# Kernel optimization log

Hardware: AMD Instinct MI355X
Metric: run time of the kernel (lower is better)

## Reference

```python
import jax, jax.numpy as jnp
import numpy as np

ALPHA = 0.2  # LeakyReLU negative slope


def setup_inputs() -> dict:
    key = jax.random.key(0)
    k1, k2, k3, k4 = jax.random.split(key, 4)
    B, N, IN, OUT = 4, 512, 128, 64
    input_feature = jax.random.normal(k1, (B, N, IN), dtype=jnp.float32)
    adj = jax.random.randint(k2, (N, N), 0, 2, dtype=jnp.int32)
    # xavier_uniform with gain=1.414 (as in torch init)
    lim_W = 1.414 * np.sqrt(6.0 / (IN + OUT))
    W = jax.random.uniform(k3, (IN, OUT), minval=-lim_W, maxval=lim_W, dtype=jnp.float32)
    lim_a = 1.414 * np.sqrt(6.0 / (2 * OUT + 1))
    a = jax.random.uniform(k4, (2 * OUT, 1), minval=-lim_a, maxval=lim_a, dtype=jnp.float32)
    return {"input_feature": input_feature, "adj": adj, "W": W, "a": a}


def reference(input_feature, adj, W, a):
    B = input_feature.shape[0]
    N = adj.shape[0]
    h = jnp.matmul(input_feature, W)              # (B, N, out)
    out = h.shape[-1]
    # Faithful replication of the torch repeat/cat(dim=1)/view pattern.
    part1 = jnp.tile(h, (1, 1, N)).reshape(B, N * N, out)  # h.repeat(1,1,N).view
    part2 = jnp.tile(h, (1, N, 1))                          # h.repeat(1,N,1)
    a_input = jnp.concatenate([part1, part2], axis=1).reshape(B, N, N, 2 * out)
    e = jax.nn.leaky_relu(jnp.squeeze(jnp.matmul(a_input, a), -1), negative_slope=ALPHA)  # (B,N,N)
    # NOTE: source overwrites the adj-masked tensor with softmax(e) — mask is dead code.
    attention = jax.nn.softmax(e, axis=2)
    # dropout is a no-op in eval mode
    h_prime = jnp.matmul(attention, h)            # (B, N, out)
    return jax.nn.elu(h_prime)                    # concat=True -> elu
```

## Files before the change

kernel.cpp:

```cpp
#include <hip/hip_runtime.h>
#include <math.h>

#define ALPHA 0.2f


#define MAGIC_ARR 0x13579BDFu
#define MAGIC_DON 0x2468ACE0u

__device__ __forceinline__ unsigned ld_acq(unsigned* p) {
    return __hip_atomic_load(p, __ATOMIC_ACQUIRE, __HIP_MEMORY_SCOPE_AGENT);
}
__device__ __forceinline__ void st_rel(unsigned* p, unsigned v) {
    __hip_atomic_store(p, v, __ATOMIC_RELEASE, __HIP_MEMORY_SCOPE_AGENT);
}
__device__ __forceinline__ void st_rlx(unsigned* p, unsigned v) {
    __hip_atomic_store(p, v, __ATOMIC_RELAXED, __HIP_MEMORY_SCOPE_AGENT);
}
__device__ __forceinline__ float ldf(float* p) {
    return __hip_atomic_load(p, __ATOMIC_RELAXED, __HIP_MEMORY_SCOPE_AGENT);
}
__device__ __forceinline__ void stf(float* p, float v) {
    __hip_atomic_store(p, v, __ATOMIC_RELAXED, __HIP_MEMORY_SCOPE_AGENT);
}

__device__ __forceinline__ void wait16(unsigned* slots, unsigned magic, int lane) {
    for (;;) {
        unsigned v = (lane < 16) ? ld_acq(&slots[lane]) : magic;
        if (__all(v == magic)) return;
        __builtin_amdgcn_s_sleep(8);
    }
}

__global__ __launch_bounds__(256) void gat_v9(
    const float* __restrict__ X, const float* __restrict__ W,
    const float* __restrict__ a, float* __restrict__ out, float* __restrict__ ws)
{
    __shared__ float XB[32][132];
    __shared__ float wa1[128], wa2[128];
    __shared__ float a_s[128];
    __shared__ float p_s[32], q_s[32];
    __shared__ float ecl[16];
    __shared__ float xs_l[3][128];
    __shared__ float Sc[3][64];
    __shared__ float zsc;

    const int tid  = threadIdx.x;
    const int lane = tid & 63;
    const int b    = blockIdx.x >> 4;
    const int r    = blockIdx.x & 15;
    const float* Xb = X + b * 65536;

    float*    wsF  = ws + b * 8192;
    unsigned* arr  = (unsigned*)wsF;
    unsigned* dn   = (unsigned*)wsF + 16;
    float*    Zp   = wsF + 32;
    float*    xs0p = wsF + 64;
    float*    xs1p = wsF + 64 + 2048;
    float*    xtp  = wsF + 64 + 4096;

    const int k2 = tid >> 1, hf = tid & 1;
    const float4* wr = (const float4*)(W + k2 * 64 + hf * 32);
    float4 wv[8];
#pragma unroll
    for (int i = 0; i < 8; ++i) wv[i] = wr[i];

    const int ra = tid >> 3, oct = tid & 7;
    const float4* xrA = (const float4*)(Xb + (32 * r + ra) * 128 + oct * 16);
    float4 xa[4];
#pragma unroll
    for (int i = 0; i < 4; ++i) xa[i] = xrA[i];

    const int gi = (ra < 16) ? (16 * r + ra) : (256 + 16 * r + (ra - 16));
    const float4* xrB = (const float4*)(Xb + gi * 128 + oct * 16);
    float4 xb[4];
#pragma unroll
    for (int i = 0; i < 4; ++i) xb[i] = xrB[i];

    if (tid < 128) a_s[tid] = a[tid];
    __syncthreads();

    {
        float r1 = 0.f, r2 = 0.f;
#pragma unroll
        for (int i = 0; i < 8; ++i) {
            const float4 w4 = wv[i];
            const int j = hf * 32 + i * 4;
            r1 = fmaf(w4.x, a_s[j],     r1); r2 = fmaf(w4.x, a_s[64 + j],     r2);
            r1 = fmaf(w4.y, a_s[j + 1], r1); r2 = fmaf(w4.y, a_s[64 + j + 1], r2);
            r1 = fmaf(w4.z, a_s[j + 2], r1); r2 = fmaf(w4.z, a_s[64 + j + 2], r2);
            r1 = fmaf(w4.w, a_s[j + 3], r1); r2 = fmaf(w4.w, a_s[64 + j + 3], r2);
        }
        r1 += __shfl_xor(r1, 1);
        r2 += __shfl_xor(r2, 1);
        if (hf == 0) { wa1[k2] = r1; wa2[k2] = r2; }
    }
#pragma unroll
    for (int i = 0; i < 4; ++i)
        *(float4*)&XB[ra][oct * 16 + i * 4] = xb[i];
    __syncthreads();

    {
        float pp = 0.f, qq = 0.f;
#pragma unroll
        for (int i = 0; i < 4; ++i) {
            const float4 x4 = xa[i];
            const int j = oct * 16 + i * 4;
            pp = fmaf(x4.x, wa1[j],     pp); qq = fmaf(x4.x, wa2[j],     qq);
            pp = fmaf(x4.y, wa1[j + 1], pp); qq = fmaf(x4.y, wa2[j + 1], qq);
            pp = fmaf(x4.z, wa1[j + 2], pp); qq = fmaf(x4.z, wa2[j + 2], qq);
            pp = fmaf(x4.w, wa1[j + 3], pp); qq = fmaf(x4.w, wa2[j + 3], qq);
        }
        pp += __shfl_xor(pp, 1); qq += __shfl_xor(qq, 1);
        pp += __shfl_xor(pp, 2); qq += __shfl_xor(qq, 2);
        pp += __shfl_xor(pp, 4); qq += __shfl_xor(qq, 4);
        if (oct == 0) { p_s[ra] = pp; q_s[ra] = qq; }
    }
    __syncthreads();

    if (tid < 16) {
        float cc = p_s[2 * tid] + q_s[2 * tid + 1];
        cc = cc > 0.f ? cc : ALPHA * cc;
        const float ecv = __expf(cc);
        ecl[tid] = ecv;
        float z = ecv;
        z += __shfl_xor(z, 1); z += __shfl_xor(z, 2);
        z += __shfl_xor(z, 4); z += __shfl_xor(z, 8);
        if (tid == 0) stf(&Zp[r], z);
    }
    __syncthreads();

    if (tid < 128) {
        const int k = tid;
        float s0 = 0.f, s1 = 0.f, st = 0.f;
#pragma unroll
        for (int i = 0; i < 16; ++i) {
            const float va = XB[i][k];
            const float vb = XB[16 + i][k];
            s0 += va; s1 += vb;
            st = fmaf(ecl[i], va + vb, st);
        }
        stf(&xs0p[r * 128 + k], s0);
        stf(&xs1p[r * 128 + k], s1);
        stf(&xtp [r * 128 + k], st);
    }
    __syncthreads();
    if (tid == 0) st_rel(&arr[r], MAGIC_ARR);

    wait16(arr, MAGIC_ARR, lane);

    if (tid < 128) {
        const int k = tid;
        float s0 = 0.f, st = 0.f;
#pragma unroll
        for (int j = 0; j < 16; ++j) s0 += ldf(&xs0p[j * 128 + k]);
#pragma unroll
        for (int j = 0; j < 16; ++j) st += ldf(&xtp[j * 128 + k]);
        xs_l[0][k] = s0;
        xs_l[2][k] = st;
    } else {
        const int k = tid - 128;
        float s1 = 0.f;
#pragma unroll
        for (int j = 0; j < 16; ++j) s1 += ldf(&xs1p[j * 128 + k]);
        xs_l[1][k] = s1;
        if (tid == 128) {
            float z = 0.f;
#pragma unroll
            for (int j = 0; j < 16; ++j) z += ldf(&Zp[j]);
            zsc = z;
        }
    }
    __syncthreads();

    {
        const int g = tid >> 6;
        if (g < 3) {
            float acc0 = 0.f, acc1 = 0.f;
#pragma unroll
            for (int k = 0; k < 128; k += 2) {
                acc0 = fmaf(xs_l[g][k],     W[k * 64 + lane],       acc0);
                acc1 = fmaf(xs_l[g][k + 1], W[(k + 1) * 64 + lane], acc1);
            }
            float acc = acc0 + acc1;
            if (g == 2) {
                acc /= (2.f * zsc);
                acc = acc > 0.f ? acc : expm1f(acc);
            }
            Sc[g][lane] = acc;
        }
    }
    __syncthreads();

    {
        const int li = tid >> 4, c4 = (tid & 15) * 4;
        float u = p_s[2 * li]     + q_s[2 * li];
        float v = p_s[2 * li + 1] + q_s[2 * li + 1];
        u = u > 0.f ? u : ALPHA * u;
        v = v > 0.f ? v : ALPHA * v;
        const float w0 = __expf(u), w1 = __expf(v);
        const float inv = 1.f / (256.f * (w0 + w1));
        const float4 s0 = *(const float4*)&Sc[0][c4];
        const float4 s1 = *(const float4*)&Sc[1][c4];
        float4 o;
        o.x = (w0 * s0.x + w1 * s1.x) * inv;
        o.y = (w0 * s0.y + w1 * s1.y) * inv;
        o.z = (w0 * s0.z + w1 * s1.z) * inv;
        o.w = (w0 * s0.w + w1 * s1.w) * inv;
        o.x = o.x > 0.f ? o.x : expm1f(o.x);
        o.y = o.y > 0.f ? o.y : expm1f(o.y);
        o.z = o.z > 0.f ? o.z : expm1f(o.z);
        o.w = o.w > 0.f ? o.w : expm1f(o.w);
        *(float4*)(out + (b * 512 + 16 * r + li) * 64 + c4) = o;
        *(float4*)(out + (b * 512 + 256 + 16 * r + li) * 64 + c4) =
            *(const float4*)&Sc[2][c4];
    }
    __syncthreads();
    if (tid == 0) st_rel(&dn[r], MAGIC_DON);

    if (r == 0 && tid < 64) {
        wait16(dn, MAGIC_DON, lane);
        if (lane < 16) { st_rlx(&arr[lane], 0u); st_rlx(&dn[lane], 0u); }
    }
}

extern "C" void kernel_launch(void* const* d_in, const int* in_sizes, int n_in,
                              void* d_out, int out_size, void* d_ws, size_t ws_size,
                              hipStream_t stream) {
    const float* X = (const float*)d_in[0];
    const float* W = (const float*)d_in[2];
    const float* a = (const float*)d_in[3];
    float* out = (float*)d_out;

    hipLaunchKernelGGL(gat_v9, dim3(64), dim3(256), 0, stream,
                       X, W, a, out, (float*)d_ws);
}
```

Baseline: 19.50 us.

## Shorten cross-block sync path with single-wave partials, vectorized gather, early release

The per-block partial sums and Z are now computed and published by one wave, which drains its stores and then releases the arrival flag. This removes the block-wide barriers before the release. Meanwhile a second wave precomputes the per-row softmax weights that later go into epw. After the wait, the workspace partials are gathered with plain float4 loads instead of scalar relaxed atomic loads. The done flag is released right after the gather, and the spin sleep is shortened. The trade-offs are more per-thread work in one wave and reliance on acquire ordering to make the plain loads coherent.

```diff
diff --git a/kernel.cpp b/kernel.cpp
--- a/kernel.cpp
+++ b/kernel.cpp
@@ -15,9 +15,6 @@
 }
 __device__ __forceinline__ void st_rlx(unsigned* p, unsigned v) {
     __hip_atomic_store(p, v, __ATOMIC_RELAXED, __HIP_MEMORY_SCOPE_AGENT);
-}
-__device__ __forceinline__ float ldf(float* p) {
-    return __hip_atomic_load(p, __ATOMIC_RELAXED, __HIP_MEMORY_SCOPE_AGENT);
 }
 __device__ __forceinline__ void stf(float* p, float v) {
     __hip_atomic_store(p, v, __ATOMIC_RELAXED, __HIP_MEMORY_SCOPE_AGENT);
@@ -27,11 +24,11 @@
     for (;;) {
         unsigned v = (lane < 16) ? ld_acq(&slots[lane]) : magic;
         if (__all(v == magic)) return;
-        __builtin_amdgcn_s_sleep(8);
-    }
-}
-
-__global__ __launch_bounds__(256) void gat_v9(
+        __builtin_amdgcn_s_sleep(1);
+    }
+}
+
+__global__ __launch_bounds__(256) void gat_v10(
     const float* __restrict__ X, const float* __restrict__ W,
     const float* __restrict__ a, float* __restrict__ out, float* __restrict__ ws)
 {
@@ -40,12 +37,13 @@
     __shared__ float a_s[128];
     __shared__ float p_s[32], q_s[32];
     __shared__ float ecl[16];
+    __shared__ float4 epw[16];
     __shared__ float xs_l[3][128];
     __shared__ float Sc[3][64];
     __shared__ float zsc;
 
     const int tid  = threadIdx.x;
-    const int lane = tid & 63;
+    const int wid  = tid >> 6, lane = tid & 63;
     const int b    = blockIdx.x >> 4;
     const int r    = blockIdx.x & 15;
     const float* Xb = X + b * 65536;
@@ -55,8 +53,6 @@
     unsigned* dn   = (unsigned*)wsF + 16;
     float*    Zp   = wsF + 32;
     float*    xs0p = wsF + 64;
-    float*    xs1p = wsF + 64 + 2048;
-    float*    xtp  = wsF + 64 + 4096;
 
     const int k2 = tid >> 1, hf = tid & 1;
     const float4* wr = (const float4*)(W + k2 * 64 + hf * 32);
@@ -117,95 +113,101 @@
     }
     __syncthreads();
 
-    if (tid < 16) {
-        float cc = p_s[2 * tid] + q_s[2 * tid + 1];
-        cc = cc > 0.f ? cc : ALPHA * cc;
-        const float ecv = __expf(cc);
-        ecl[tid] = ecv;
+    if (wid == 0) {
+        float ecv = 0.f;
+        if (lane < 16) {
+            float cc = p_s[2 * lane] + q_s[2 * lane + 1];
+            cc = cc > 0.f ? cc : ALPHA * cc;
+            ecv = __expf(cc);
+            ecl[lane] = ecv;
+        }
         float z = ecv;
         z += __shfl_xor(z, 1); z += __shfl_xor(z, 2);
         z += __shfl_xor(z, 4); z += __shfl_xor(z, 8);
-        if (tid == 0) stf(&Zp[r], z);
-    }
-    __syncthreads();
-
-    if (tid < 128) {
-        const int k = tid;
-        float s0 = 0.f, s1 = 0.f, st = 0.f;
+        if (lane == 0) stf(&Zp[r], z);
+
+        float s0a = 0.f, s1a = 0.f, sta = 0.f;
+        float s0b = 0.f, s1b = 0.f, stb = 0.f;
 #pragma unroll
         for (int i = 0; i < 16; ++i) {
-            const float va = XB[i][k];
-            const float vb = XB[16 + i][k];
-            s0 += va; s1 += vb;
-            st = fmaf(ecl[i], va + vb, st);
-        }
-        stf(&xs0p[r * 128 + k], s0);
-        stf(&xs1p[r * 128 + k], s1);
-        stf(&xtp [r * 128 + k], st);
-    }
-    __syncthreads();
-    if (tid == 0) st_rel(&arr[r], MAGIC_ARR);
-
-    wait16(arr, MAGIC_ARR, lane);
-
-    if (tid < 128) {
-        const int k = tid;
-        float s0 = 0.f, st = 0.f;
-#pragma unroll
-        for (int j = 0; j < 16; ++j) s0 += ldf(&xs0p[j * 128 + k]);
-#pragma unroll
-        for (int j = 0; j < 16; ++j) st += ldf(&xtp[j * 128 + k]);
-        xs_l[0][k] = s0;
-        xs_l[2][k] = st;
-    } else {
-        const int k = tid - 128;
-        float s1 = 0.f;
-#pragma unroll
-        for (int j = 0; j < 16; ++j) s1 += ldf(&xs1p[j * 128 + k]);
-        xs_l[1][k] = s1;
-        if (tid == 128) {
-            float z = 0.f;
-#pragma unroll
-            for (int j = 0; j < 16; ++j) z += ldf(&Zp[j]);
-            zsc = z;
-        }
-    }
-    __syncthreads();
-
-    {
-        const int g = tid >> 6;
-        if (g < 3) {
-            float acc0 = 0.f, acc1 = 0.f;
-#pragma unroll
-            for (int k = 0; k < 128; k += 2) {
-                acc0 = fmaf(xs_l[g][k],     W[k * 64 + lane],       acc0);
-                acc1 = fmaf(xs_l[g][k + 1], W[(k + 1) * 64 + lane], acc1);
-            }
-            float acc = acc0 + acc1;
-            if (g == 2) {
-                acc /= (2.f * zsc);
-                acc = acc > 0.f ? acc : expm1f(acc);
-            }
-            Sc[g][lane] = acc;
-        }
-    }
-    __syncthreads();
-
-    {
-        const int li = tid >> 4, c4 = (tid & 15) * 4;
+            const float e  = ecl[i];
+            const float va = XB[i][lane],      vb = XB[16 + i][lane];
+            const float wa = XB[i][lane + 64], wb = XB[16 + i][lane + 64];
+            s0a += va; s1a += vb; sta = fmaf(e, va + vb, sta);
+            s0b += wa; s1b += wb; stb = fmaf(e, wa + wb, stb);
+        }
+        stf(&xs0p[r * 128 + lane],             s0a);
+        stf(&xs0p[r * 128 + lane + 64],        s0b);
+        stf(&xs0p[2048 + r * 128 + lane],      s1a);
+        stf(&xs0p[2048 + r * 128 + lane + 64], s1b);
+        stf(&xs0p[4096 + r * 128 + lane],      sta);
+        stf(&xs0p[4096 + r * 128 + lane + 64], stb);
+        asm volatile("s_waitcnt vmcnt(0)" ::: "memory");
+        __builtin_amdgcn_sched_barrier(0);
+        if (lane == 0) st_rel(&arr[r], MAGIC_ARR);
+    } else if (tid >= 64 && tid < 80) {
+        const int li = tid - 64;
         float u = p_s[2 * li]     + q_s[2 * li];
         float v = p_s[2 * li + 1] + q_s[2 * li + 1];
         u = u > 0.f ? u : ALPHA * u;
         v = v > 0.f ? v : ALPHA * v;
         const float w0 = __expf(u), w1 = __expf(v);
-        const float inv = 1.f / (256.f * (w0 + w1));
+        float4 e;
+        e.x = w0; e.y = w1; e.z = 1.f / (256.f * (w0 + w1)); e.w = 0.f;
+        epw[li] = e;
+    }
+
+    wait16(arr, MAGIC_ARR, lane);
+
+    if (tid < 96) {
+        const int g = tid >> 5, k4 = tid & 31;
+        const float4* src = (const float4*)(xs0p + g * 2048) + k4;
+        float4 s; s.x = 0.f; s.y = 0.f; s.z = 0.f; s.w = 0.f;
+#pragma unroll
+        for (int j = 0; j < 16; ++j) {
+            const float4 v = src[j * 32];
+            s.x += v.x; s.y += v.y; s.z += v.z; s.w += v.w;
+        }
+        *(float4*)&xs_l[g][4 * k4] = s;
+    } else if (tid == 96) {
+        float z = 0.f;
+#pragma unroll
+        for (int j = 0; j < 16; ++j) z += Zp[j];
+        zsc = z;
+    }
+    __syncthreads();
+
+    if (tid == 0) st_rel(&dn[r], MAGIC_DON);
+
+    if (tid < 192) {
+        const int g = wid;
+        float a0 = 0.f, a1 = 0.f, a2 = 0.f, a3 = 0.f;
+#pragma unroll
+        for (int k = 0; k < 128; k += 4) {
+            a0 = fmaf(xs_l[g][k],     W[(k)     * 64 + lane], a0);
+            a1 = fmaf(xs_l[g][k + 1], W[(k + 1) * 64 + lane], a1);
+            a2 = fmaf(xs_l[g][k + 2], W[(k + 2) * 64 + lane], a2);
+            a3 = fmaf(xs_l[g][k + 3], W[(k + 3) * 64 + lane], a3);
+        }
+        float acc = (a0 + a1) + (a2 + a3);
+        if (g == 2) {
+            acc /= (2.f * zsc);
+            acc = acc > 0.f ? acc : expm1f(acc);
+        }
+        Sc[g][lane] = acc;
+    }
+    __syncthreads();
+
+    {
+        const int li = tid >> 4, c4 = (tid & 15) << 2;
+        const float4 e  = epw[li];
         const float4 s0 = *(const float4*)&Sc[0][c4];
         const float4 s1 = *(const float4*)&Sc[1][c4];
         float4 o;
-        o.x = (w0 * s0.x + w1 * s1.x) * inv;
-        o.y = (w0 * s0.y + w1 * s1.y) * inv;
-        o.z = (w0 * s0.z + w1 * s1.z) * inv;
-        o.w = (w0 * s0.w + w1 * s1.w) * inv;
+        o.x = (e.x * s0.x + e.y * s1.x) * e.z;
+        o.y = (e.x * s0.y + e.y * s1.y) * e.z;
+        o.z = (e.x * s0.z + e.y * s1.z) * e.z;
+        o.w = (e.x * s0.w + e.y * s1.w) * e.z;
         o.x = o.x > 0.f ? o.x : expm1f(o.x);
         o.y = o.y > 0.f ? o.y : expm1f(o.y);
         o.z = o.z > 0.f ? o.z : expm1f(o.z);
@@ -214,10 +216,8 @@
         *(float4*)(out + (b * 512 + 256 + 16 * r + li) * 64 + c4) =
             *(const float4*)&Sc[2][c4];
     }
-    __syncthreads();
-    if (tid == 0) st_rel(&dn[r], MAGIC_DON);
-
-    if (r == 0 && tid < 64) {
+
+    if (r == 0 && wid == 0) {
         wait16(dn, MAGIC_DON, lane);
         if (lane < 16) { st_rlx(&arr[lane], 0u); st_rlx(&dn[lane], 0u); }
     }
@@ -231,6 +231,6 @@
     const float* a = (const float*)d_in[3];
     float* out = (float*)d_out;
 
-    hipLaunchKernelGGL(gat_v9, dim3(64), dim3(256), 0, stream,
+    hipLaunchKernelGGL(gat_v10, dim3(64), dim3(256), 0, stream,
                        X, W, a, out, (float*)d_ws);
 }
```

Result: slower. 21.96 us (+12.6%).
